# Kernel optimization log

Measured on AMD Instinct MI355X. Metric: run time of the kernel, lower is better.

Reference implementation:

```python
import jax, jax.numpy as jnp
import numpy as np
from jax import lax

C = 768
CA = C // 4  # adapter_channels = 192
L = 197      # 1 CLS + 14*14 patches
T_FRAMES = 16
B = 16
N = B * T_FRAMES


def quick_gelu(x):
    return x * jax.nn.sigmoid(1.702 * x)


def setup_inputs() -> dict:
    key = jax.random.key(0)
    ks = jax.random.split(key, 16)
    s = 0.02
    return {
        "x": jax.random.normal(ks[0], (L, N, C), dtype=jnp.float32),
        "T": T_FRAMES,
        # main path (fc1 -> depthwise conv1d over T -> fc2)
        "fc1_w": jax.random.normal(ks[1], (C, CA), jnp.float32) * s,
        "fc1_b": jnp.zeros((CA,), jnp.float32),
        "conv_w": jax.random.normal(ks[2], (CA, 1, 3), jnp.float32) * s,  # (O, I/g, K)
        "conv_b": jnp.zeros((CA,), jnp.float32),
        "fc2_w": jax.random.normal(ks[3], (CA, C), jnp.float32) * s,
        "fc2_b": jnp.zeros((C,), jnp.float32),
        # offset adapter (fc1 -> depthwise conv3d (1,3,3) -> fc2)
        "off_fc1_w": jax.random.normal(ks[4], (C, CA), jnp.float32) * s,
        "off_fc1_b": jnp.zeros((CA,), jnp.float32),
        "off_conv_w": jax.random.normal(ks[5], (CA, 1, 1, 3, 3), jnp.float32) * s,  # (O, I/g, D, H, W)
        "off_conv_b": jnp.zeros((CA,), jnp.float32),
        "off_fc2_w": jax.random.normal(ks[6], (CA, C), jnp.float32) * s,
        "off_fc2_b": jnp.zeros((C,), jnp.float32),
        # mlp branch (c_in -> QuickGELU -> c_out)
        "mlp_in_w": jax.random.normal(ks[7], (C, CA), jnp.float32) * s,
        "mlp_in_b": jnp.zeros((CA,), jnp.float32),
        "mlp_out_w": jax.random.normal(ks[8], (CA, C), jnp.float32) * s,
        "mlp_out_b": jnp.zeros((C,), jnp.float32),
    }


def _offset_adapter(x, T, fc1_w, fc1_b, conv_w, conv_b, fc2_w, fc2_b):
    Lx, Nx, Cx = x.shape
    Bx = Nx // T
    HW = Lx - 1
    H = int(round(HW ** 0.5))
    Ca = fc1_w.shape[1]
    xp = jnp.transpose(x, (1, 0, 2))            # (N, L, C)
    xs = xp[:, 1:, :].reshape(Bx, T, HW, Cx)    # (B, T, HW, C)
    # former frame: index [0, 0, 1, ..., T-2]
    x_former = jnp.concatenate([xs[:, :1], xs[:, :-1]], axis=1)
    off = xs - x_former
    off = off @ fc1_w + fc1_b                   # (B, T, HW, Ca)
    off = off.reshape(Bx, T, H, H, Ca).transpose(0, 4, 1, 2, 3)  # (B, Ca, T, H, W)
    off = lax.conv_general_dilated(
        off, conv_w, window_strides=(1, 1, 1),
        padding=[(0, 0), (1, 1), (1, 1)],
        dimension_numbers=("NCDHW", "OIDHW", "NCDHW"),
        feature_group_count=Ca,
    ) + conv_b[None, :, None, None, None]
    off = off.transpose(0, 2, 3, 4, 1).reshape(Nx, HW, Ca)
    off = off @ fc2_w + fc2_b                   # (N, L-1, C)
    return jnp.transpose(off, (1, 0, 2))        # (L-1, N, C)


def reference(x, T, fc1_w, fc1_b, conv_w, conv_b, fc2_w, fc2_b,
              off_fc1_w, off_fc1_b, off_conv_w, off_conv_b, off_fc2_w, off_fc2_b,
              mlp_in_w, mlp_in_b, mlp_out_w, mlp_out_b):
    Lx, Nx, Cx = x.shape
    Bx = Nx // T
    Ca = fc1_w.shape[1]

    offset = _offset_adapter(x, T, off_fc1_w, off_fc1_b, off_conv_w, off_conv_b,
                             off_fc2_w, off_fc2_b)  # (L-1, N, C)

    # mlp identity branch
    x_id = quick_gelu(x @ mlp_in_w + mlp_in_b) @ mlp_out_w + mlp_out_b  # (L, N, C)

    # main branch: fc1 -> depthwise conv1d along T -> fc2
    h = x @ fc1_w + fc1_b                                   # (L, N, Ca)
    h = jnp.transpose(h, (1, 0, 2)).reshape(Bx, T, Lx, Ca)  # (B, T, L, Ca)
    h = h.transpose(0, 2, 3, 1).reshape(Bx * Lx, Ca, T)     # (B*L, Ca, T)
    h = lax.conv_general_dilated(
        h, conv_w, window_strides=(1,), padding=[(1, 1)],
        dimension_numbers=("NCH", "OIH", "NCH"),
        feature_group_count=Ca,
    ) + conv_b[None, :, None]
    h = h.transpose(0, 2, 1).reshape(Bx, Lx, T, Ca)
    h = h.transpose(0, 2, 1, 3).reshape(Nx, Lx, Ca)
    h = jnp.transpose(h, (1, 0, 2))                         # (L, N, Ca)
    h = h @ fc2_w + fc2_b                                   # (L, N, C)

    x_id = x_id.at[1:].add(offset)
    return h + x_id
```

## Files before the change

kernel.cpp:

```cpp
#include <hip/hip_runtime.h>

#define L_DIM 197
#define N_DIM 256
#define C_DIM 768
#define CA_DIM 192
#define M_DIM (L_DIM * N_DIM)

typedef short s16x8 __attribute__((ext_vector_type(8)));
typedef float f32x4 __attribute__((ext_vector_type(4)));

__device__ __forceinline__ unsigned short f2bf(float f) {
  unsigned x = __builtin_bit_cast(unsigned, f);
  x = (x + 0x7fffu + ((x >> 16) & 1u)) >> 16;
  return (unsigned short)x;
}
__device__ __forceinline__ float bflo(unsigned u) { return __builtin_bit_cast(float, u << 16); }
__device__ __forceinline__ float bfhi(unsigned u) { return __builtin_bit_cast(float, u & 0xffff0000u); }

__device__ __forceinline__ void unp8(uint4 v, float* f) {
  f[0] = bflo(v.x); f[1] = bfhi(v.x); f[2] = bflo(v.y); f[3] = bfhi(v.y);
  f[4] = bflo(v.z); f[5] = bfhi(v.z); f[6] = bflo(v.w); f[7] = bfhi(v.w);
}

__device__ __forceinline__ unsigned cvtpk(float lo, float hi) {
  unsigned r;
  asm("v_cvt_pk_bf16_f32 %0, %1, %2" : "=v"(r) : "v"(lo), "v"(hi));
  return r;
}

__device__ __forceinline__ void mfma16(f32x4& acc, s16x8 a, s16x8 b) {
  asm("v_mfma_f32_16x16x32_bf16 %0, %1, %2, %0" : "+v"(acc) : "v"(a), "v"(b));
}

typedef const void __attribute__((address_space(1)))* gp_t;
typedef void __attribute__((address_space(3)))* lp_t;
__device__ __forceinline__ void gl16(const void* g, void* l) {
  __builtin_amdgcn_global_load_lds((gp_t)g, (lp_t)l, 16, 0, 0);
}

#define WAITVM(n) asm volatile("s_waitcnt vmcnt(" #n ")" ::: "memory")
#define BARRIER_LG() asm volatile("s_waitcnt lgkmcnt(0)\ns_barrier" ::: "memory")

__device__ __forceinline__ int swz(int pid, int nwg) {
  const int q = nwg >> 3, r = nwg & 7, x = pid & 7, s = pid >> 3;
  return (x < r ? x * (q + 1) : r * (q + 1) + (x - r) * q) + s;
}

__global__ __launch_bounds__(256) void prep_k(
    const float* __restrict__ fc1_w, const float* __restrict__ mlp_in_w,
    const float* __restrict__ off_fc1_w, const float* __restrict__ fc2_w,
    const float* __restrict__ mlp_out_w, const float* __restrict__ off_fc2_w,
    unsigned short* __restrict__ wa, unsigned short* __restrict__ wc) {
  __shared__ float t[32][33];
  const int b = blockIdx.x;
  const int job = b / 144, tt = b - job * 144;
  const float* in = job == 0 ? fc1_w : job == 1 ? mlp_in_w : job == 2 ? off_fc1_w
                  : job == 3 ? fc2_w : job == 4 ? mlp_out_w : off_fc2_w;
  const int Cc = job < 3 ? 192 : 768;
  const int tc = Cc >> 5;
  const int tr0 = (tt / tc) << 5, tc0 = (tt - (tt / tc) * tc) << 5;
  const int lr = threadIdx.x >> 5, lc = threadIdx.x & 31;
#pragma unroll
  for (int p = 0; p < 4; p++)
    t[p * 8 + lr][lc] = in[(tr0 + p * 8 + lr) * Cc + tc0 + lc];
  __syncthreads();
#pragma unroll
  for (int p = 0; p < 4; p++) {
    const int orow = tc0 + p * 8 + lr;
    const int ocol = tr0 + lc;
    const unsigned short v = f2bf(t[lc][p * 8 + lr]);
    if (job < 3) wa[(job * 192 + orow) * 768 + ocol] = v;
    else         wc[orow * 576 + (job - 3) * 192 + ocol] = v;
  }
}

__global__ __launch_bounds__(256, 1) void gemm_a_k(
    const float* __restrict__ x, const unsigned short* __restrict__ wa,
    const float* __restrict__ fc1_b, const float* __restrict__ mlp_in_b,
    const float* __restrict__ cw, const float* __restrict__ cb,
    const float* __restrict__ off_b1, unsigned short* __restrict__ hcat) {
  __shared__ unsigned short As[3][128 * 32];
  __shared__ unsigned short Bs[3][192 * 32];
  const int tid = threadIdx.x, lane = tid & 63, w = tid >> 6;
  const int lid = swz(blockIdx.x, 3 * 394);
  const int by = lid / 3, bx = lid - by * 3;
  const int m0 = by * 128, n0 = bx * 192;

  const int sr = tid >> 2, sc8 = (tid & 3) * 8;
  const float* gA = x + (size_t)(m0 + sr) * C_DIM + sc8;
  const unsigned short* gB = wa + (size_t)(n0 + sr) * C_DIM + sc8;

  float4 avA[4], avB[4];
  auto ldA = [&](int kt, float4* av) {
    const float* p = gA + kt * 32;
    av[0] = *(const float4*)p;                  av[1] = *(const float4*)(p + 4);
    av[2] = *(const float4*)(p + 64 * C_DIM);   av[3] = *(const float4*)(p + 64 * C_DIM + 4);
  };
  auto wrA = [&](int b, const float4* av) {
    uint4 u0, u1;
    u0.x = cvtpk(av[0].x, av[0].y); u0.y = cvtpk(av[0].z, av[0].w);
    u0.z = cvtpk(av[1].x, av[1].y); u0.w = cvtpk(av[1].z, av[1].w);
    u1.x = cvtpk(av[2].x, av[2].y); u1.y = cvtpk(av[2].z, av[2].w);
    u1.z = cvtpk(av[3].x, av[3].y); u1.w = cvtpk(av[3].z, av[3].w);
    *(uint4*)&As[b][sr * 32 + sc8] = u0;
    *(uint4*)&As[b][(64 + sr) * 32 + sc8] = u1;
  };
  auto stB = [&](int kt, int b) {
    const unsigned short* pb = gB + kt * 32;
    gl16(pb,               &Bs[b][sr * 32 + sc8]);
    gl16(pb + 64 * C_DIM,  &Bs[b][(64 + sr) * 32 + sc8]);
    gl16(pb + 128 * C_DIM, &Bs[b][(128 + sr) * 32 + sc8]);
  };

  f32x4 acc[4][6];
#pragma unroll
  for (int i = 0; i < 4; i++)
#pragma unroll
    for (int j = 0; j < 6; j++) acc[i][j] = (f32x4){0.f, 0.f, 0.f, 0.f};

  const int fr = lane & 15, fq = lane >> 4;
  const int wm = (w >> 1) * 64, wn = (w & 1) * 96;

  ldA(0, avA);
  stB(0, 0);
  ldA(1, avB);
  WAITVM(7);
  wrA(0, avA);

#pragma unroll 6
  for (int kt = 0; kt < 24; ++kt) {
    const int b = kt % 3;
    float4* ldset = ((kt & 1) == 0) ? avA : avB;
    float4* wrset = ((kt & 1) == 0) ? avB : avA;
    if (kt + 2 < 24) ldA(kt + 2, ldset);
    if (kt + 1 < 24) stB(kt + 1, (kt + 1) % 3);
    if (kt < 22)      { WAITVM(7); }
    else if (kt == 22){ WAITVM(3); }
    else              { WAITVM(0); }
    if (kt + 1 < 24) wrA((kt + 1) % 3, wrset);
    BARRIER_LG();
    s16x8 af[4], bfv[6];
#pragma unroll
    for (int mi = 0; mi < 4; mi++)
      af[mi] = *(const s16x8*)&As[b][(wm + mi * 16 + fr) * 32 + fq * 8];
#pragma unroll
    for (int ni = 0; ni < 6; ni++)
      bfv[ni] = *(const s16x8*)&Bs[b][(wn + ni * 16 + fr) * 32 + fq * 8];
#pragma unroll
    for (int mi = 0; mi < 4; mi++)
#pragma unroll
      for (int ni = 0; ni < 6; ni++) mfma16(acc[mi][ni], af[mi], bfv[ni]);
  }

  if (bx == 0) {
#pragma unroll
    for (int ni = 0; ni < 6; ni++) {
      const int ca = wn + ni * 16 + fr;
      const float bv = fc1_b[ca];
      const float w0 = cw[ca * 3], w1 = cw[ca * 3 + 1], w2 = cw[ca * 3 + 2];
      const float cbv = cb[ca];
#pragma unroll
      for (int mi = 0; mi < 4; mi++) {
        const float v0 = acc[mi][ni][0] + bv, v1 = acc[mi][ni][1] + bv;
        const float v2 = acc[mi][ni][2] + bv, v3 = acc[mi][ni][3] + bv;
        const float pv3 = __shfl_up(v3, 16);
        const float nv0 = __shfl_down(v0, 16);
        const float p0 = fq > 0 ? pv3 : 0.f;
        const float n3 = fq < 3 ? nv0 : 0.f;
        const int mb = m0 + wm + mi * 16 + fq * 4;
        hcat[(size_t)(mb + 0) * 576 + ca] = f2bf(w0 * p0 + w1 * v0 + w2 * v1 + cbv);
        hcat[(size_t)(mb + 1) * 576 + ca] = f2bf(w0 * v0 + w1 * v1 + w2 * v2 + cbv);
        hcat[(size_t)(mb + 2) * 576 + ca] = f2bf(w0 * v1 + w1 * v2 + w2 * v3 + cbv);
        hcat[(size_t)(mb + 3) * 576 + ca] = f2bf(w0 * v2 + w1 * v3 + w2 * n3 + cbv);
      }
    }
  } else if (bx == 1) {
#pragma unroll
    for (int ni = 0; ni < 6; ni++) {
      const int ca = wn + ni * 16 + fr;
      const float bv = mlp_in_b[ca];
#pragma unroll
      for (int mi = 0; mi < 4; mi++)
#pragma unroll
        for (int r = 0; r < 4; r++) {
          const int m = m0 + wm + mi * 16 + fq * 4 + r;
          float v = acc[mi][ni][r] + bv;
          v = v / (1.f + __expf(-1.702f * v));
          hcat[(size_t)m * 576 + 192 + ca] = f2bf(v);
        }
    }
  } else {
    const bool zrow = (by < 2);
#pragma unroll
    for (int ni = 0; ni < 6; ni++) {
      const int ca = wn + ni * 16 + fr;
      const float bv = off_b1[ca];
#pragma unroll
      for (int mi = 0; mi < 4; mi++) {
        const float v0 = acc[mi][ni][0], v1 = acc[mi][ni][1];
        const float v2 = acc[mi][ni][2], v3 = acc[mi][ni][3];
        const float pv3 = __shfl_up(v3, 16);
        const int mb = m0 + wm + mi * 16 + fq * 4;
        const float o0 = (fq == 0) ? bv : (v0 - pv3 + bv);
        if (zrow) {
          hcat[(size_t)(mb + 0) * 576 + 384 + ca] = 0;
          hcat[(size_t)(mb + 1) * 576 + 384 + ca] = 0;
          hcat[(size_t)(mb + 2) * 576 + 384 + ca] = 0;
          hcat[(size_t)(mb + 3) * 576 + 384 + ca] = 0;
        } else {
          hcat[(size_t)(mb + 0) * 576 + 384 + ca] = f2bf(o0);
          hcat[(size_t)(mb + 1) * 576 + 384 + ca] = f2bf(v1 - v0 + bv);
          hcat[(size_t)(mb + 2) * 576 + 384 + ca] = f2bf(v2 - v1 + bv);
          hcat[(size_t)(mb + 3) * 576 + 384 + ca] = f2bf(v3 - v2 + bv);
        }
      }
    }
  }
}

__global__ __launch_bounds__(256) void conv3d_k(
    const float* __restrict__ w3, const float* __restrict__ b2,
    unsigned short* __restrict__ hcat) {
  __shared__ float ds[196 * 48];
  __shared__ float w3s[9 * 48];
  __shared__ float b2s[48];
  const int blk = blockIdx.x;
  const int n = blk >> 2, q = blk & 3;
  const int ch0 = q * 48;
  const int tid = threadIdx.x;

  for (int j = tid; j < 432; j += 256) {
    const int c = j / 9, tap = j % 9;
    w3s[tap * 48 + c] = w3[(ch0 + c) * 9 + tap];
  }
  if (tid < 48) b2s[tid] = b2[ch0 + tid];

  for (int j = tid; j < 196 * 6; j += 256) {
    const int hw = j / 6, ck = j % 6;
    float dv[8];
    unp8(*(const uint4*)(hcat + ((size_t)(1 + hw) * 256 + n) * 576 + 384 + ch0 + ck * 8), dv);
#pragma unroll
    for (int e = 0; e < 8; e++) ds[hw * 48 + ck * 8 + e] = dv[e];
  }
  __syncthreads();

  for (int j = tid; j < 196 * 6; j += 256) {
    const int hw = j / 6, ck = j % 6;
    const int i = hw / 14, j0 = hw - i * 14;
    float acc[8];
#pragma unroll
    for (int e = 0; e < 8; e++) acc[e] = b2s[ck * 8 + e];
#pragma unroll
    for (int di = 0; di < 3; di++) {
      const int ii = i + di - 1;
      if (ii < 0 || ii >= 14) continue;
#pragma unroll
      for (int dj = 0; dj < 3; dj++) {
        const int jc = j0 + dj - 1;
        if (jc < 0 || jc >= 14) continue;
        const float* dp = &ds[(ii * 14 + jc) * 48 + ck * 8];
        const float* wp = &w3s[(di * 3 + dj) * 48 + ck * 8];
#pragma unroll
        for (int e = 0; e < 8; e++) acc[e] += wp[e] * dp[e];
      }
    }
    unsigned o[4];
#pragma unroll
    for (int e = 0; e < 8; e += 2)
      o[e / 2] = (unsigned)f2bf(acc[e]) | ((unsigned)f2bf(acc[e + 1]) << 16);
    uint4 ov; ov.x = o[0]; ov.y = o[1]; ov.z = o[2]; ov.w = o[3];
    *(uint4*)(hcat + ((size_t)(1 + hw) * 256 + n) * 576 + 384 + ch0 + ck * 8) = ov;
  }
}

__global__ __launch_bounds__(256, 1) void gemm_c_k(
    const unsigned short* __restrict__ hcat, const unsigned short* __restrict__ wc,
    const float* __restrict__ fc2_b, const float* __restrict__ mlp_out_b,
    const float* __restrict__ off_fc2_b, float* __restrict__ out) {
  __shared__ unsigned short As[3][128 * 32];
  __shared__ unsigned short Bs[3][256 * 32];
  const int tid = threadIdx.x, lane = tid & 63, w = tid >> 6;
  const int lid = swz(blockIdx.x, 3 * 394);
  const int by = lid / 3, bx = lid - by * 3;
  const int m0 = by * 128, n0 = bx * 256;

  const int sr = tid >> 2, sc = (tid & 3) * 8;
  const unsigned short* gA = hcat + (size_t)(m0 + sr) * 576 + sc;
  const unsigned short* gB = wc + (size_t)(n0 + sr) * 576 + sc;
  auto stage = [&](int kt, int b) {
#pragma unroll
    for (int j = 0; j < 2; j++)
      gl16(gA + kt * 32 + j * 64 * 576, &As[b][(sr + j * 64) * 32 + sc]);
#pragma unroll
    for (int j = 0; j < 4; j++)
      gl16(gB + kt * 32 + j * 64 * 576, &Bs[b][(sr + j * 64) * 32 + sc]);
  };

  f32x4 acc[4][8];
#pragma unroll
  for (int i = 0; i < 4; i++)
#pragma unroll
    for (int j = 0; j < 8; j++) acc[i][j] = (f32x4){0.f, 0.f, 0.f, 0.f};

  const int fr = lane & 15, fq = lane >> 4;
  const int wm = (w >> 1) * 64, wn = (w & 1) * 128;

  stage(0, 0);
#pragma unroll 3
  for (int kt = 0; kt < 18; ++kt) {
    const int b = kt % 3;
    if (kt + 1 < 18) { stage(kt + 1, (kt + 1) % 3); WAITVM(6); }
    else             { WAITVM(0); }
    __builtin_amdgcn_s_barrier();
    asm volatile("" ::: "memory");
    s16x8 af[4], bfv[8];
#pragma unroll
    for (int mi = 0; mi < 4; mi++)
      af[mi] = *(const s16x8*)&As[b][(wm + mi * 16 + fr) * 32 + fq * 8];
#pragma unroll
    for (int ni = 0; ni < 8; ni++)
      bfv[ni] = *(const s16x8*)&Bs[b][(wn + ni * 16 + fr) * 32 + fq * 8];
#pragma unroll
    for (int mi = 0; mi < 4; mi++)
#pragma unroll
      for (int ni = 0; ni < 8; ni++) mfma16(acc[mi][ni], af[mi], bfv[ni]);
  }

  float bv[8];
#pragma unroll
  for (int ni = 0; ni < 8; ni++) {
    const int c = n0 + wn + ni * 16 + fr;
    bv[ni] = fc2_b[c] + mlp_out_b[c] + (by >= 2 ? off_fc2_b[c] : 0.f);
  }
#pragma unroll
  for (int mi = 0; mi < 4; mi++)
#pragma unroll
    for (int r = 0; r < 4; r++) {
      const int m = m0 + wm + mi * 16 + fq * 4 + r;
      float* op = out + (size_t)m * C_DIM + n0 + wn;
#pragma unroll
      for (int ni = 0; ni < 8; ni++) op[ni * 16 + fr] = acc[mi][ni][r] + bv[ni];
    }
}

extern "C" void kernel_launch(void* const* d_in, const int* in_sizes, int n_in,
                              void* d_out, int out_size, void* d_ws, size_t ws_size,
                              hipStream_t stream) {
  const float* x          = (const float*)d_in[0];
  const float* fc1_w      = (const float*)d_in[2];
  const float* fc1_b      = (const float*)d_in[3];
  const float* conv_w     = (const float*)d_in[4];
  const float* conv_b     = (const float*)d_in[5];
  const float* fc2_w      = (const float*)d_in[6];
  const float* fc2_b      = (const float*)d_in[7];
  const float* off_fc1_w  = (const float*)d_in[8];
  const float* off_fc1_b  = (const float*)d_in[9];
  const float* off_conv_w = (const float*)d_in[10];
  const float* off_conv_b = (const float*)d_in[11];
  const float* off_fc2_w  = (const float*)d_in[12];
  const float* off_fc2_b  = (const float*)d_in[13];
  const float* mlp_in_w   = (const float*)d_in[14];
  const float* mlp_in_b   = (const float*)d_in[15];
  const float* mlp_out_w  = (const float*)d_in[16];
  const float* mlp_out_b  = (const float*)d_in[17];
  float* out = (float*)d_out;

  char* ws = (char*)d_ws;
  unsigned short* hcat = (unsigned short*)(ws);
  unsigned short* wa   = (unsigned short*)(ws + (size_t)M_DIM * 576 * 2);
  unsigned short* wc   = wa + (size_t)576 * 768;

  prep_k<<<864, 256, 0, stream>>>(fc1_w, mlp_in_w, off_fc1_w, fc2_w, mlp_out_w,
                                  off_fc2_w, wa, wc);
  gemm_a_k<<<1182, 256, 0, stream>>>(x, wa, fc1_b, mlp_in_b, conv_w, conv_b,
                                     off_fc1_b, hcat);
  conv3d_k<<<1024, 256, 0, stream>>>(off_conv_w, off_conv_b, hcat);
  gemm_c_k<<<1182, 256, 0, stream>>>(hcat, wc, fc2_b, mlp_out_b, off_fc2_b, out);
}
```

Before: 204.1 us.

## Stage fp32 A tile via direct global-to-LDS loads and convert at fragment read

The A operand (fp32 activations) is now loaded straight into shared memory with global_load_lds instead of through registers. It is converted to bf16 only when each wave reads its MFMA fragments. The pipeline drops from a triple-buffered register/LDS scheme with explicit vmcnt waits to a double buffer with __syncthreads per iteration. This frees registers and removes the register round trip, but it doubles A's LDS footprint and bandwidth, repeats conversion work across waves, and may expose load latency because the waits are coarser.

```diff
diff --git a/kernel.cpp b/kernel.cpp
--- a/kernel.cpp
+++ b/kernel.cpp
@@ -27,6 +27,12 @@
   asm("v_cvt_pk_bf16_f32 %0, %1, %2" : "=v"(r) : "v"(lo), "v"(hi));
   return r;
 }
+__device__ __forceinline__ s16x8 cvt8(float4 p0, float4 p1) {
+  uint4 u;
+  u.x = cvtpk(p0.x, p0.y); u.y = cvtpk(p0.z, p0.w);
+  u.z = cvtpk(p1.x, p1.y); u.w = cvtpk(p1.z, p1.w);
+  return __builtin_bit_cast(s16x8, u);
+}
 
 __device__ __forceinline__ void mfma16(f32x4& acc, s16x8 a, s16x8 b) {
   asm("v_mfma_f32_16x16x32_bf16 %0, %1, %2, %0" : "+v"(acc) : "v"(a), "v"(b));
@@ -39,7 +45,6 @@
 }
 
 #define WAITVM(n) asm volatile("s_waitcnt vmcnt(" #n ")" ::: "memory")
-#define BARRIER_LG() asm volatile("s_waitcnt lgkmcnt(0)\ns_barrier" ::: "memory")
 
 __device__ __forceinline__ int swz(int pid, int nwg) {
   const int q = nwg >> 3, r = nwg & 7, x = pid & 7, s = pid >> 3;
@@ -79,37 +84,27 @@
     const float* __restrict__ fc1_b, const float* __restrict__ mlp_in_b,
     const float* __restrict__ cw, const float* __restrict__ cb,
     const float* __restrict__ off_b1, unsigned short* __restrict__ hcat) {
-  __shared__ unsigned short As[3][128 * 32];
-  __shared__ unsigned short Bs[3][192 * 32];
+  __shared__ float Asf[2][128 * 32];
+  __shared__ unsigned short Bs[2][192 * 32];
   const int tid = threadIdx.x, lane = tid & 63, w = tid >> 6;
   const int lid = swz(blockIdx.x, 3 * 394);
   const int by = lid / 3, bx = lid - by * 3;
   const int m0 = by * 128, n0 = bx * 192;
 
-  const int sr = tid >> 2, sc8 = (tid & 3) * 8;
-  const float* gA = x + (size_t)(m0 + sr) * C_DIM + sc8;
-  const unsigned short* gB = wa + (size_t)(n0 + sr) * C_DIM + sc8;
-
-  float4 avA[4], avB[4];
-  auto ldA = [&](int kt, float4* av) {
-    const float* p = gA + kt * 32;
-    av[0] = *(const float4*)p;                  av[1] = *(const float4*)(p + 4);
-    av[2] = *(const float4*)(p + 64 * C_DIM);   av[3] = *(const float4*)(p + 64 * C_DIM + 4);
-  };
-  auto wrA = [&](int b, const float4* av) {
-    uint4 u0, u1;
-    u0.x = cvtpk(av[0].x, av[0].y); u0.y = cvtpk(av[0].z, av[0].w);
-    u0.z = cvtpk(av[1].x, av[1].y); u0.w = cvtpk(av[1].z, av[1].w);
-    u1.x = cvtpk(av[2].x, av[2].y); u1.y = cvtpk(av[2].z, av[2].w);
-    u1.z = cvtpk(av[3].x, av[3].y); u1.w = cvtpk(av[3].z, av[3].w);
-    *(uint4*)&As[b][sr * 32 + sc8] = u0;
-    *(uint4*)&As[b][(64 + sr) * 32 + sc8] = u1;
-  };
-  auto stB = [&](int kt, int b) {
+  const int ar = tid >> 3, ac4 = (tid & 7) * 4;
+  const float* gA = x + (size_t)(m0 + ar) * C_DIM + ac4;
+  const int br = tid >> 2, bc8 = (tid & 3) * 8;
+  const unsigned short* gB = wa + (size_t)(n0 + br) * C_DIM + bc8;
+
+  auto stage = [&](int kt, int b) {
+    const float* pa = gA + kt * 32;
+#pragma unroll
+    for (int j = 0; j < 4; j++)
+      gl16(pa + (size_t)j * 32 * C_DIM, &Asf[b][(j * 32 + ar) * 32 + ac4]);
     const unsigned short* pb = gB + kt * 32;
-    gl16(pb,               &Bs[b][sr * 32 + sc8]);
-    gl16(pb + 64 * C_DIM,  &Bs[b][(64 + sr) * 32 + sc8]);
-    gl16(pb + 128 * C_DIM, &Bs[b][(128 + sr) * 32 + sc8]);
+#pragma unroll
+    for (int j = 0; j < 3; j++)
+      gl16(pb + (size_t)j * 64 * C_DIM, &Bs[b][(j * 64 + br) * 32 + bc8]);
   };
 
   f32x4 acc[4][6];
@@ -121,28 +116,19 @@
   const int fr = lane & 15, fq = lane >> 4;
   const int wm = (w >> 1) * 64, wn = (w & 1) * 96;
 
-  ldA(0, avA);
-  stB(0, 0);
-  ldA(1, avB);
-  WAITVM(7);
-  wrA(0, avA);
-
-#pragma unroll 6
+  stage(0, 0);
+  __syncthreads();
+#pragma unroll 2
   for (int kt = 0; kt < 24; ++kt) {
-    const int b = kt % 3;
-    float4* ldset = ((kt & 1) == 0) ? avA : avB;
-    float4* wrset = ((kt & 1) == 0) ? avB : avA;
-    if (kt + 2 < 24) ldA(kt + 2, ldset);
-    if (kt + 1 < 24) stB(kt + 1, (kt + 1) % 3);
-    if (kt < 22)      { WAITVM(7); }
-    else if (kt == 22){ WAITVM(3); }
-    else              { WAITVM(0); }
-    if (kt + 1 < 24) wrA((kt + 1) % 3, wrset);
-    BARRIER_LG();
+    const int b = kt & 1;
+    if (kt + 1 < 24) stage(kt + 1, b ^ 1);
+    const float4* Af = (const float4*)&Asf[b][0];
     s16x8 af[4], bfv[6];
 #pragma unroll
-    for (int mi = 0; mi < 4; mi++)
-      af[mi] = *(const s16x8*)&As[b][(wm + mi * 16 + fr) * 32 + fq * 8];
+    for (int mi = 0; mi < 4; mi++) {
+      const int row = wm + mi * 16 + fr;
+      af[mi] = cvt8(Af[row * 8 + fq * 2], Af[row * 8 + fq * 2 + 1]);
+    }
 #pragma unroll
     for (int ni = 0; ni < 6; ni++)
       bfv[ni] = *(const s16x8*)&Bs[b][(wn + ni * 16 + fr) * 32 + fq * 8];
@@ -150,6 +136,7 @@
     for (int mi = 0; mi < 4; mi++)
 #pragma unroll
       for (int ni = 0; ni < 6; ni++) mfma16(acc[mi][ni], af[mi], bfv[ni]);
+    __syncthreads();
   }
 
   if (bx == 0) {
```

New measurement: 211.0 us. 3.4% more time.
